# Kernel tuning notes

Measured on AMD Instinct MI355X. Metric: run time of the kernel, lower is better.

Reference implementation:

```python
import jax, jax.numpy as jnp
import numpy as np

DIM = 768
NUM_HEADS = 8
HEAD_DIM = DIM // NUM_HEADS
SCALE = HEAD_DIM ** -0.5


def setup_inputs() -> dict:
    key = jax.random.key(0)
    k1, k2, k3, k4 = jax.random.split(key, 4)
    B, C, H, W = 8, DIM, 32, 32
    x = jax.random.normal(k1, (B, C, H, W), dtype=jnp.float32)
    # torch Linear stores weight as (out, in); y = x @ W.T + b
    w_qkv = jax.random.normal(k2, (3 * DIM, DIM), dtype=jnp.float32) * (DIM ** -0.5)
    w_proj = jax.random.normal(k3, (DIM, DIM), dtype=jnp.float32) * (DIM ** -0.5)
    b_proj = jax.random.normal(k4, (DIM,), dtype=jnp.float32) * 0.02
    return {"x": x, "w_qkv": w_qkv, "w_proj": w_proj, "b_proj": b_proj}


def reference(x, w_qkv, w_proj, b_proj):
    B, C, H, W = x.shape
    N = H * W
    nh, hd = NUM_HEADS, HEAD_DIM
    # (B, C, H, W) -> (B, N, C)
    tokens = x.reshape(B, C, N).transpose(0, 2, 1)
    qkv = tokens @ w_qkv.T  # (B, N, 3C), no bias (qkv_bias=False)
    qkv = qkv.reshape(B, N, 3, nh, hd).transpose(2, 0, 3, 1, 4)  # (3, B, nh, N, hd)
    q, k, v = qkv[0], qkv[1], qkv[2]
    attn = jnp.einsum('bhnd,bhmd->bhnm', q, k) * SCALE
    attn = jax.nn.softmax(attn, axis=-1)  # attn_drop=0.0 (eval)
    out = jnp.einsum('bhnm,bhmd->bhnd', attn, v)  # (B, nh, N, hd)
    out = out.transpose(0, 2, 1, 3).reshape(B, N, C)
    out = out @ w_proj.T + b_proj  # proj_drop=0.0
    return out.transpose(0, 2, 1).reshape(B, C, H, W)
```

## Files before the change

### kernel.cpp

```cpp
#include <hip/hip_runtime.h>

typedef short s16x8 __attribute__((ext_vector_type(8)));
typedef short s16x4 __attribute__((ext_vector_type(4)));
typedef float f32x4 __attribute__((ext_vector_type(4)));
typedef int   i32x4 __attribute__((ext_vector_type(4)));
typedef unsigned u32x2 __attribute__((ext_vector_type(2)));

#define SCALE_F 0.10206207261596577f
#define KLOG2E  0.14724444f
#define DEFER_THR 11.5415603f

__device__ __forceinline__ unsigned short f2bf(float f) {
  unsigned u = __builtin_bit_cast(unsigned, f);
  u += 0x7fffu + ((u >> 16) & 1u);
  return (unsigned short)(u >> 16);
}
__device__ __forceinline__ unsigned cvt_pk_bf16(float a, float b) {
  unsigned r;
  asm("v_cvt_pk_bf16_f32 %0, %1, %2" : "=v"(r) : "v"(a), "v"(b));
  return r;
}
__device__ __forceinline__ float exp2_fast(float x) {
  float r;
  asm("v_exp_f32 %0, %1" : "=v"(r) : "v"(x));
  return r;
}

#define MFMA16(a, b, c) __builtin_amdgcn_mfma_f32_16x16x32_bf16((a), (b), (c), 0, 0, 0)

__device__ __forceinline__ void gl_lds16(const unsigned short* g, unsigned short* l) {
  __builtin_amdgcn_global_load_lds(
      (const __attribute__((address_space(1))) void*)g,
      (__attribute__((address_space(3))) void*)l, 16, 0, 0);
}

__global__ __launch_bounds__(256) void cvt_bf16_kernel(const float* __restrict__ src,
                                                       unsigned short* __restrict__ dst, int n4) {
  int i = blockIdx.x * 256 + threadIdx.x;
  if (i >= n4) return;
  f32x4 v = reinterpret_cast<const f32x4*>(src)[i];
  s16x4 o;
  o[0] = (short)f2bf(v[0]); o[1] = (short)f2bf(v[1]);
  o[2] = (short)f2bf(v[2]); o[3] = (short)f2bf(v[3]);
  reinterpret_cast<s16x4*>(dst)[i] = o;
}

__global__ __launch_bounds__(256) void transpose_x_kernel(const float* __restrict__ x,
                                                          unsigned short* __restrict__ tokens) {
  __shared__ float t[32][33];
  const int ct = blockIdx.x * 32, nt = blockIdx.y * 32, b = blockIdx.z;
  const int tx = threadIdx.x, ty = threadIdx.y;
  const float* xp = x + (size_t)b * 768 * 1024;
#pragma unroll
  for (int r = 0; r < 4; ++r) {
    int c = ty + r * 8;
    t[c][tx] = xp[(size_t)(ct + c) * 1024 + nt + tx];
  }
  __syncthreads();
  unsigned short* tp = tokens + (size_t)b * 1024 * 768;
#pragma unroll
  for (int r = 0; r < 4; ++r) {
    int n = ty + r * 8;
    tp[(size_t)(nt + n) * 768 + ct + tx] = f2bf(t[tx][n]);
  }
}

__global__ __launch_bounds__(512, 4) void qkv_gemm_kernel(const unsigned short* __restrict__ A,
                                                          const unsigned short* __restrict__ Bt,
                                                          unsigned short* __restrict__ Qo,
                                                          unsigned short* __restrict__ Ko,
                                                          unsigned short* __restrict__ Vt) {
  __shared__ unsigned short lds[36864];
  const int tid = threadIdx.x;
  const int wave = tid >> 6, lane = tid & 63;
  const int wm = wave >> 1, wn = wave & 1;
  const int lr = lane & 15, lg = lane >> 4;
  const int bid = blockIdx.x;
  const int xcd = bid & 7, idx = bid >> 3;
  const int m0 = (xcd * 4 + idx / 18) * 256;
  const int n0 = (idx % 18) * 128;

  const int srow = tid >> 2, sslot = tid & 3;

  f32x4 acc[4][4] = {};

#define STAGE_KT(ktv, bb)                                                       \
  {                                                                             \
    unsigned short* lb = lds + (bb) * 12288;                                    \
    _Pragma("unroll")                                                           \
    for (int rr = 0; rr < 2; ++rr) {                                            \
      const int row = rr * 128 + srow;                                          \
      const int c = sslot ^ ((row >> 1) & 3);                                   \
      gl_lds16(A + (size_t)(m0 + row) * 768 + (ktv) * 32 + c * 8,               \
               lb + rr * 4096 + wave * 512);                                    \
    }                                                                           \
    {                                                                           \
      const int c = sslot ^ ((srow >> 1) & 3);                                  \
      gl_lds16(Bt + (size_t)(n0 + srow) * 768 + (ktv) * 32 + c * 8,             \
               lb + 8192 + wave * 512);                                         \
    }                                                                           \
  }

  STAGE_KT(0, 0)
  STAGE_KT(1, 1)
  asm volatile("s_waitcnt vmcnt(3)" ::: "memory");
  __builtin_amdgcn_s_barrier();

  int cb = 0;
  for (int kt = 0; kt < 24; ++kt) {
    unsigned short* curb = lds + cb * 12288;
    s16x8 af[4], bf[4];
#pragma unroll
    for (int mi = 0; mi < 4; ++mi) {
      const int row = wm * 64 + mi * 16 + lr;
      af[mi] = *reinterpret_cast<const s16x8*>(
          &curb[row * 32 + ((lg ^ ((row >> 1) & 3)) * 8)]);
    }
#pragma unroll
    for (int ni = 0; ni < 4; ++ni) {
      const int row = wn * 64 + ni * 16 + lr;
      bf[ni] = *reinterpret_cast<const s16x8*>(
          &curb[8192 + row * 32 + ((lg ^ ((row >> 1) & 3)) * 8)]);
    }
    if (kt < 22) {
      const int sb = (cb == 0) ? 2 : cb - 1;
      STAGE_KT(kt + 2, sb)
    }
    __builtin_amdgcn_s_barrier();
    asm volatile("s_waitcnt lgkmcnt(0)" ::: "memory");
    __builtin_amdgcn_sched_barrier(0);
    __builtin_amdgcn_s_setprio(1);
#pragma unroll
    for (int mi = 0; mi < 4; ++mi)
#pragma unroll
      for (int ni = 0; ni < 4; ++ni)
        acc[mi][ni] = MFMA16(af[mi], bf[ni], acc[mi][ni]);
    __builtin_amdgcn_s_setprio(0);
    if (kt < 22) {
      asm volatile("s_waitcnt vmcnt(3)" ::: "memory");
    } else if (kt == 22) {
      asm volatile("s_waitcnt vmcnt(0)" ::: "memory");
    }
    __builtin_amdgcn_s_barrier();
    cb = (cb == 2) ? 0 : cb + 1;
  }
#undef STAGE_KT

  const int colbase = n0 + wn * 64;
  const int ttype = colbase / 768;
  if (ttype == 2) {
#pragma unroll
    for (int ni = 0; ni < 4; ++ni) {
      const int cc = colbase + ni * 16 + lr - 2 * 768;
      const int h = cc / 96, d = cc - h * 96;
#pragma unroll
      for (int mi = 0; mi < 4; ++mi) {
        const int gm = m0 + wm * 64 + mi * 16 + lg * 4;
        const int b = gm >> 10, n = gm & 1023;
        const int np = (n & ~31) | (((n >> 2) & 3) << 3) | (((n >> 4) & 1) << 2);
        u32x2 p2;
        p2[0] = cvt_pk_bf16(acc[mi][ni][0], acc[mi][ni][1]);
        p2[1] = cvt_pk_bf16(acc[mi][ni][2], acc[mi][ni][3]);
        *reinterpret_cast<s16x4*>(Vt + ((size_t)(b * 8 + h) * 96 + d) * 1024 + np) =
            __builtin_bit_cast(s16x4, p2);
      }
    }
  } else {
    unsigned short* W = lds + wave * 4096;
    unsigned short* dstbuf = (ttype == 0) ? Qo : Ko;
#pragma unroll
    for (int mi = 0; mi < 4; ++mi)
#pragma unroll
      for (int ni = 0; ni < 4; ++ni) {
        const int cc = ni * 16 + lr;
        const int ch = cc >> 3, wi = cc & 7;
#pragma unroll
        for (int j = 0; j < 4; ++j) {
          const int r = mi * 16 + lg * 4 + j;
          W[r * 64 + ((ch ^ (r & 7)) * 8) + wi] = f2bf(acc[mi][ni][j]);
        }
      }
    asm volatile("s_waitcnt lgkmcnt(0)" ::: "memory");
    __builtin_amdgcn_sched_barrier(0);
#pragma unroll
    for (int i = 0; i < 8; ++i) {
      const int r = i * 8 + (lane >> 3), c = lane & 7;
      s16x8 v8 = *reinterpret_cast<const s16x8*>(&W[r * 64 + ((c ^ (r & 7)) * 8)]);
      const int cc = colbase + c * 8 - ttype * 768;
      const int h = cc / 96, d = cc - h * 96;
      const int gm = m0 + wm * 64 + r;
      const int b = gm >> 10, n = gm & 1023;
      *reinterpret_cast<s16x8*>(dstbuf + ((size_t)(b * 8 + h) * 1024 + n) * 96 + d) = v8;
    }
  }
}

__device__ __forceinline__ void stage128(const unsigned short* __restrict__ A,
                                         const unsigned short* __restrict__ Bt,
                                         unsigned short* lA, unsigned short* lB,
                                         int m0, int n0, int k0, int tid, int wave) {
  const int r2 = tid >> 2, s = tid & 3;
#pragma unroll
  for (int i = 0; i < 2; ++i) {
    const int row = i * 64 + r2;
    const int c = s ^ ((row >> 1) & 3);
    gl_lds16(A + (size_t)(m0 + row) * 768 + k0 + c * 8, lA + i * 2048 + wave * 512);
    gl_lds16(Bt + (size_t)(n0 + row) * 768 + k0 + c * 8, lB + i * 2048 + wave * 512);
  }
}

#define GEMM128_LOOP(A, Bt)                                                             \
  stage128(A, Bt, lA, lB, m0, n0, 0, tid, wave);                                        \
  __syncthreads();                                                                      \
  for (int t = 0; t < 24; ++t) {                                                        \
    const int cur = t & 1;                                                              \
    if (t < 23)                                                                         \
      stage128(A, Bt, lA + (cur ^ 1) * 4096, lB + (cur ^ 1) * 4096, m0, n0,             \
               (t + 1) * 32, tid, wave);                                                \
    s16x8 af[4], bf[4];                                                                 \
    _Pragma("unroll")                                                                   \
    for (int mi = 0; mi < 4; ++mi) {                                                    \
      const int row = wr * 64 + mi * 16 + lr;                                           \
      af[mi] = *reinterpret_cast<const s16x8*>(                                         \
          &lA[cur * 4096 + row * 32 + ((lg ^ ((row >> 1) & 3)) * 8)]);                  \
    }                                                                                   \
    _Pragma("unroll")                                                                   \
    for (int ni = 0; ni < 4; ++ni) {                                                    \
      const int row = wc * 64 + ni * 16 + lr;                                           \
      bf[ni] = *reinterpret_cast<const s16x8*>(                                         \
          &lB[cur * 4096 + row * 32 + ((lg ^ ((row >> 1) & 3)) * 8)]);                  \
    }                                                                                   \
    _Pragma("unroll")                                                                   \
    for (int mi = 0; mi < 4; ++mi)                                                      \
      _Pragma("unroll")                                                                 \
      for (int ni = 0; ni < 4; ++ni)                                                    \
        acc[mi][ni] = MFMA16(af[mi], bf[ni], acc[mi][ni]);                              \
    __syncthreads();                                                                    \
  }

__global__ __launch_bounds__(256, 4) void proj_gemm_kernel(const unsigned short* __restrict__ A,
                                                           const unsigned short* __restrict__ Bt,
                                                           const float* __restrict__ bias,
                                                           float* __restrict__ out) {
  __shared__ unsigned short lds_all[16384];
  unsigned short* lA = lds_all;
  unsigned short* lB = lds_all + 8192;

  const int tid = threadIdx.x;
  const int wave = tid >> 6, lane = tid & 63;
  const int wr = wave >> 1, wc = wave & 1;
  const int lr = lane & 15, lg = lane >> 4;
  const int bid = blockIdx.x;
  const int xcd = bid & 7, idx = bid >> 3;
  const int m0 = (xcd * 8 + idx / 6) * 128;
  const int n0 = (idx % 6) * 128;

  f32x4 acc[4][4] = {};
  GEMM128_LOOP(A, Bt)

#pragma unroll
  for (int ni = 0; ni < 4; ++ni) {
    const int col = n0 + wc * 64 + ni * 16 + lr;
    const float bv = bias[col];
#pragma unroll
    for (int mi = 0; mi < 4; ++mi) {
      const int gm = m0 + wr * 64 + mi * 16 + lg * 4;
      const int b = gm >> 10, n = gm & 1023;
      f32x4 v;
#pragma unroll
      for (int j = 0; j < 4; ++j) v[j] = acc[mi][ni][j] + bv;
      *reinterpret_cast<f32x4*>(out + (size_t)b * 768 * 1024 + (size_t)col * 1024 + n) = v;
    }
  }
}

__global__ __launch_bounds__(512, 4) void attn_kernel(const unsigned short* __restrict__ Q,
                                                      const unsigned short* __restrict__ K,
                                                      const unsigned short* __restrict__ Vt,
                                                      unsigned short* __restrict__ Ao) {
  __shared__ unsigned short lds[2][12288];

  const int f = blockIdx.x;
  const int xcd = f & 7;
  const int g = (f >> 3) + xcd * 64;
  const int bh = g >> 3, qb = g & 7;

  const int tid = threadIdx.x, wave = tid >> 6, lane = tid & 63;
  const int lr = lane & 15, lg = lane >> 4;
  const int klo = (lr >> 1) & 3;

  const unsigned short* Qp = Q + (size_t)bh * 1024 * 96;
  const unsigned short* Kp = K + (size_t)bh * 1024 * 96;
  const unsigned short* Vp = Vt + (size_t)bh * 96 * 1024;

  const int qrow = qb * 128 + wave * 16 + lr;
  s16x8 qreg[3];
#pragma unroll
  for (int kd = 0; kd < 3; ++kd)
    qreg[kd] = *reinterpret_cast<const s16x8*>(Qp + (size_t)qrow * 96 + kd * 32 + lg * 8);

  float m2 = -1e30f, l_r = 0.f;
  f32x4 oacc[6] = {};

#define STAGE(bufi, kv0)                                                              \
  {                                                                                   \
    _Pragma("unroll")                                                                 \
    for (int i = 0; i < 3; ++i) {                                                     \
      const int wl = wave + 8 * i;                                                    \
      if (wl < 12) {                                                                  \
        const int kd = wl >> 2, rg = wl & 3;                                          \
        const int row = rg * 16 + (lane >> 2);                                        \
        const int c8 = (lane & 3) ^ ((row >> 1) & 3);                                 \
        gl_lds16(Kp + (size_t)((kv0) + row) * 96 + kd * 32 + c8 * 8,                  \
                 &lds[bufi][0] + kd * 2048 + rg * 512);                               \
      } else {                                                                        \
        const int v = wl - 12;                                                        \
        const int gs = v / 6, rg = v - gs * 6;                                        \
        const int drow = rg * 16 + (lane >> 2);                                       \
        const int c8 = (lane & 3) ^ ((drow >> 1) & 3);                                \
        gl_lds16(Vp + (size_t)drow * 1024 + (kv0) + gs * 32 + c8 * 8,                 \
                 &lds[bufi][0] + 6144 + gs * 3072 + rg * 512);                        \
      }                                                                               \
    }                                                                                 \
  }

  STAGE(0, 0);
  __syncthreads();

  for (int gt = 0; gt < 16; ++gt) {
    const int buf = gt & 1;
    if (gt < 15) STAGE(buf ^ 1, (gt + 1) * 64);

    f32x4 sacc[4] = {};
    __builtin_amdgcn_s_setprio(1);
#pragma unroll
    for (int c = 0; c < 4; ++c) {
#pragma unroll
      for (int kd = 0; kd < 3; ++kd) {
        s16x8 kf = *reinterpret_cast<const s16x8*>(
            &lds[buf][kd * 2048 + (c * 16 + lr) * 32 + ((lg ^ klo) * 8)]);
        sacc[c] = MFMA16(kf, qreg[kd], sacc[c]);
      }
    }
    __builtin_amdgcn_s_setprio(0);

    float mx = fmaxf(fmaxf(sacc[0][0], sacc[0][1]), fmaxf(sacc[0][2], sacc[0][3]));
#pragma unroll
    for (int c = 1; c < 4; ++c)
      mx = fmaxf(mx, fmaxf(fmaxf(sacc[c][0], sacc[c][1]), fmaxf(sacc[c][2], sacc[c][3])));
    mx = fmaxf(mx, __shfl_xor(mx, 16));
    mx = fmaxf(mx, __shfl_xor(mx, 32));
    const float mc = mx * KLOG2E;
    if (!__all(mc - m2 <= DEFER_THR)) {
      const float m2n = fmaxf(m2, mc);
      const float rsc = exp2_fast(m2 - m2n);
      l_r *= rsc;
#pragma unroll
      for (int dt = 0; dt < 6; ++dt) oacc[dt] *= rsc;
      m2 = m2n;
    }
    float ts = 0.f;
    unsigned pk[4][2];
#pragma unroll
    for (int c = 0; c < 4; ++c) {
      float p0 = exp2_fast(__builtin_fmaf(sacc[c][0], KLOG2E, -m2));
      float p1 = exp2_fast(__builtin_fmaf(sacc[c][1], KLOG2E, -m2));
      float p2 = exp2_fast(__builtin_fmaf(sacc[c][2], KLOG2E, -m2));
      float p3 = exp2_fast(__builtin_fmaf(sacc[c][3], KLOG2E, -m2));
      ts += (p0 + p1) + (p2 + p3);
      pk[c][0] = cvt_pk_bf16(p0, p1);
      pk[c][1] = cvt_pk_bf16(p2, p3);
    }
    ts += __shfl_xor(ts, 16);
    ts += __shfl_xor(ts, 32);
    l_r += ts;

    __builtin_amdgcn_s_setprio(1);
#pragma unroll
    for (int gs = 0; gs < 2; ++gs) {
      i32x4 bi;
      bi[0] = (int)pk[2 * gs][0];
      bi[1] = (int)pk[2 * gs][1];
      bi[2] = (int)pk[2 * gs + 1][0];
      bi[3] = (int)pk[2 * gs + 1][1];
      s16x8 pf = __builtin_bit_cast(s16x8, bi);
#pragma unroll
      for (int dt = 0; dt < 6; ++dt) {
        s16x8 vf = *reinterpret_cast<const s16x8*>(
            &lds[buf][6144 + gs * 3072 + (dt * 16 + lr) * 32 + ((lg ^ klo) * 8)]);
        oacc[dt] = MFMA16(vf, pf, oacc[dt]);
      }
    }
    __builtin_amdgcn_s_setprio(0);
    __syncthreads();
  }

  const float invl = 1.0f / l_r;
  const int b_ = bh >> 3, h_ = bh & 7;
  unsigned short* orow = Ao + (size_t)(b_ * 1024 + qrow) * 768 + h_ * 96;
#pragma unroll
  for (int dt = 0; dt < 6; ++dt) {
    u32x2 p2;
    p2[0] = cvt_pk_bf16(oacc[dt][0] * invl, oacc[dt][1] * invl);
    p2[1] = cvt_pk_bf16(oacc[dt][2] * invl, oacc[dt][3] * invl);
    *reinterpret_cast<s16x4*>(orow + dt * 16 + lg * 4) = __builtin_bit_cast(s16x4, p2);
  }
#undef STAGE
}

extern "C" void kernel_launch(void* const* d_in, const int* in_sizes, int n_in,
                              void* d_out, int out_size, void* d_ws, size_t ws_size,
                              hipStream_t stream) {
  const float* x = (const float*)d_in[0];
  const float* wqkv = (const float*)d_in[1];
  const float* wproj = (const float*)d_in[2];
  const float* bproj = (const float*)d_in[3];
  float* out = (float*)d_out;

  unsigned short* ws = (unsigned short*)d_ws;
  unsigned short* tokens = ws;
  unsigned short* wqkv_b = tokens + 8192 * 768;
  unsigned short* wproj_b = wqkv_b + 2304 * 768;
  unsigned short* Qb = wproj_b + 768 * 768;
  unsigned short* Kb = Qb + 64 * 1024 * 96;
  unsigned short* Vb = Kb + 64 * 1024 * 96;
  unsigned short* Ab = Vb + 64 * 1024 * 96;

  cvt_bf16_kernel<<<1728, 256, 0, stream>>>(wqkv, wqkv_b, 2304 * 768 / 4);
  cvt_bf16_kernel<<<576, 256, 0, stream>>>(wproj, wproj_b, 768 * 768 / 4);
  transpose_x_kernel<<<dim3(24, 32, 8), dim3(32, 8), 0, stream>>>(x, tokens);
  qkv_gemm_kernel<<<576, 512, 0, stream>>>(tokens, wqkv_b, Qb, Kb, Vb);
  attn_kernel<<<512, 512, 0, stream>>>(Qb, Kb, Vb, Ab);
  proj_gemm_kernel<<<384, 256, 0, stream>>>(Ab, wproj_b, bproj, out);
}
```

Before: 116.7 us.

## Process two query tiles per wave in attention to reuse K/V fragments

```diff
diff --git a/kernel.cpp b/kernel.cpp
--- a/kernel.cpp
+++ b/kernel.cpp
@@ -209,35 +209,6 @@
   }
 }
 
-#define GEMM128_LOOP(A, Bt)                                                             \
-  stage128(A, Bt, lA, lB, m0, n0, 0, tid, wave);                                        \
-  __syncthreads();                                                                      \
-  for (int t = 0; t < 24; ++t) {                                                        \
-    const int cur = t & 1;                                                              \
-    if (t < 23)                                                                         \
-      stage128(A, Bt, lA + (cur ^ 1) * 4096, lB + (cur ^ 1) * 4096, m0, n0,             \
-               (t + 1) * 32, tid, wave);                                                \
-    s16x8 af[4], bf[4];                                                                 \
-    _Pragma("unroll")                                                                   \
-    for (int mi = 0; mi < 4; ++mi) {                                                    \
-      const int row = wr * 64 + mi * 16 + lr;                                           \
-      af[mi] = *reinterpret_cast<const s16x8*>(                                         \
-          &lA[cur * 4096 + row * 32 + ((lg ^ ((row >> 1) & 3)) * 8)]);                  \
-    }                                                                                   \
-    _Pragma("unroll")                                                                   \
-    for (int ni = 0; ni < 4; ++ni) {                                                    \
-      const int row = wc * 64 + ni * 16 + lr;                                           \
-      bf[ni] = *reinterpret_cast<const s16x8*>(                                         \
-          &lB[cur * 4096 + row * 32 + ((lg ^ ((row >> 1) & 3)) * 8)]);                  \
-    }                                                                                   \
-    _Pragma("unroll")                                                                   \
-    for (int mi = 0; mi < 4; ++mi)                                                      \
-      _Pragma("unroll")                                                                 \
-      for (int ni = 0; ni < 4; ++ni)                                                    \
-        acc[mi][ni] = MFMA16(af[mi], bf[ni], acc[mi][ni]);                              \
-    __syncthreads();                                                                    \
-  }
-
 __global__ __launch_bounds__(256, 4) void proj_gemm_kernel(const unsigned short* __restrict__ A,
                                                            const unsigned short* __restrict__ Bt,
                                                            const float* __restrict__ bias,
@@ -256,7 +227,33 @@
   const int n0 = (idx % 6) * 128;
 
   f32x4 acc[4][4] = {};
-  GEMM128_LOOP(A, Bt)
+  stage128(A, Bt, lA, lB, m0, n0, 0, tid, wave);
+  __syncthreads();
+  for (int t = 0; t < 24; ++t) {
+    const int cur = t & 1;
+    if (t < 23)
+      stage128(A, Bt, lA + (cur ^ 1) * 4096, lB + (cur ^ 1) * 4096, m0, n0,
+               (t + 1) * 32, tid, wave);
+    s16x8 af[4], bf[4];
+#pragma unroll
+    for (int mi = 0; mi < 4; ++mi) {
+      const int row = wr * 64 + mi * 16 + lr;
+      af[mi] = *reinterpret_cast<const s16x8*>(
+          &lA[cur * 4096 + row * 32 + ((lg ^ ((row >> 1) & 3)) * 8)]);
+    }
+#pragma unroll
+    for (int ni = 0; ni < 4; ++ni) {
+      const int row = wc * 64 + ni * 16 + lr;
+      bf[ni] = *reinterpret_cast<const s16x8*>(
+          &lB[cur * 4096 + row * 32 + ((lg ^ ((row >> 1) & 3)) * 8)]);
+    }
+#pragma unroll
+    for (int mi = 0; mi < 4; ++mi)
+#pragma unroll
+      for (int ni = 0; ni < 4; ++ni)
+        acc[mi][ni] = MFMA16(af[mi], bf[ni], acc[mi][ni]);
+    __syncthreads();
+  }
 
 #pragma unroll
   for (int ni = 0; ni < 4; ++ni) {
@@ -274,7 +271,7 @@
   }
 }
 
-__global__ __launch_bounds__(512, 4) void attn_kernel(const unsigned short* __restrict__ Q,
+__global__ __launch_bounds__(256, 2) void attn_kernel(const unsigned short* __restrict__ Q,
                                                       const unsigned short* __restrict__ K,
                                                       const unsigned short* __restrict__ Vt,
                                                       unsigned short* __restrict__ Ao) {
@@ -293,20 +290,23 @@
   const unsigned short* Kp = K + (size_t)bh * 1024 * 96;
   const unsigned short* Vp = Vt + (size_t)bh * 96 * 1024;
 
-  const int qrow = qb * 128 + wave * 16 + lr;
-  s16x8 qreg[3];
-#pragma unroll
-  for (int kd = 0; kd < 3; ++kd)
-    qreg[kd] = *reinterpret_cast<const s16x8*>(Qp + (size_t)qrow * 96 + kd * 32 + lg * 8);
-
-  float m2 = -1e30f, l_r = 0.f;
-  f32x4 oacc[6] = {};
+  s16x8 qreg[3][2];
+#pragma unroll
+  for (int u = 0; u < 2; ++u) {
+    const int qrow = qb * 128 + wave * 32 + u * 16 + lr;
+#pragma unroll
+    for (int kd = 0; kd < 3; ++kd)
+      qreg[kd][u] = *reinterpret_cast<const s16x8*>(Qp + (size_t)qrow * 96 + kd * 32 + lg * 8);
+  }
+
+  float m2[2] = {-1e30f, -1e30f}, l_r[2] = {0.f, 0.f};
+  f32x4 oacc[6][2] = {};
 
 #define STAGE(bufi, kv0)                                                              \
   {                                                                                   \
     _Pragma("unroll")                                                                 \
-    for (int i = 0; i < 3; ++i) {                                                     \
-      const int wl = wave + 8 * i;                                                    \
+    for (int i = 0; i < 6; ++i) {                                                     \
+      const int wl = wave + 4 * i;                                                    \
       if (wl < 12) {                                                                  \
         const int kd = wl >> 2, rg = wl & 3;                                          \
         const int row = rg * 16 + (lane >> 2);                                        \
@@ -331,79 +331,97 @@
     const int buf = gt & 1;
     if (gt < 15) STAGE(buf ^ 1, (gt + 1) * 64);
 
-    f32x4 sacc[4] = {};
+    f32x4 sacc[4][2] = {};
     __builtin_amdgcn_s_setprio(1);
 #pragma unroll
     for (int c = 0; c < 4; ++c) {
-#pragma unroll
-      for (int kd = 0; kd < 3; ++kd) {
-        s16x8 kf = *reinterpret_cast<const s16x8*>(
+      s16x8 kf[3];
+#pragma unroll
+      for (int kd = 0; kd < 3; ++kd)
+        kf[kd] = *reinterpret_cast<const s16x8*>(
             &lds[buf][kd * 2048 + (c * 16 + lr) * 32 + ((lg ^ klo) * 8)]);
-        sacc[c] = MFMA16(kf, qreg[kd], sacc[c]);
-      }
+#pragma unroll
+      for (int kd = 0; kd < 3; ++kd)
+#pragma unroll
+        for (int u = 0; u < 2; ++u)
+          sacc[c][u] = MFMA16(kf[kd], qreg[kd][u], sacc[c][u]);
     }
     __builtin_amdgcn_s_setprio(0);
 
-    float mx = fmaxf(fmaxf(sacc[0][0], sacc[0][1]), fmaxf(sacc[0][2], sacc[0][3]));
-#pragma unroll
-    for (int c = 1; c < 4; ++c)
-      mx = fmaxf(mx, fmaxf(fmaxf(sacc[c][0], sacc[c][1]), fmaxf(sacc[c][2], sacc[c][3])));
-    mx = fmaxf(mx, __shfl_xor(mx, 16));
-    mx = fmaxf(mx, __shfl_xor(mx, 32));
-    const float mc = mx * KLOG2E;
-    if (!__all(mc - m2 <= DEFER_THR)) {
-      const float m2n = fmaxf(m2, mc);
-      const float rsc = exp2_fast(m2 - m2n);
-      l_r *= rsc;
-#pragma unroll
-      for (int dt = 0; dt < 6; ++dt) oacc[dt] *= rsc;
-      m2 = m2n;
-    }
-    float ts = 0.f;
-    unsigned pk[4][2];
-#pragma unroll
-    for (int c = 0; c < 4; ++c) {
-      float p0 = exp2_fast(__builtin_fmaf(sacc[c][0], KLOG2E, -m2));
-      float p1 = exp2_fast(__builtin_fmaf(sacc[c][1], KLOG2E, -m2));
-      float p2 = exp2_fast(__builtin_fmaf(sacc[c][2], KLOG2E, -m2));
-      float p3 = exp2_fast(__builtin_fmaf(sacc[c][3], KLOG2E, -m2));
-      ts += (p0 + p1) + (p2 + p3);
-      pk[c][0] = cvt_pk_bf16(p0, p1);
-      pk[c][1] = cvt_pk_bf16(p2, p3);
-    }
-    ts += __shfl_xor(ts, 16);
-    ts += __shfl_xor(ts, 32);
-    l_r += ts;
+    unsigned pk[2][4][2];
+#pragma unroll
+    for (int u = 0; u < 2; ++u) {
+      float mx = fmaxf(fmaxf(sacc[0][u][0], sacc[0][u][1]), fmaxf(sacc[0][u][2], sacc[0][u][3]));
+#pragma unroll
+      for (int c = 1; c < 4; ++c)
+        mx = fmaxf(mx, fmaxf(fmaxf(sacc[c][u][0], sacc[c][u][1]),
+                             fmaxf(sacc[c][u][2], sacc[c][u][3])));
+      mx = fmaxf(mx, __shfl_xor(mx, 16));
+      mx = fmaxf(mx, __shfl_xor(mx, 32));
+      const float mc = mx * KLOG2E;
+      if (!__all(mc - m2[u] <= DEFER_THR)) {
+        const float m2n = fmaxf(m2[u], mc);
+        const float rsc = exp2_fast(m2[u] - m2n);
+        l_r[u] *= rsc;
+#pragma unroll
+        for (int dt = 0; dt < 6; ++dt) oacc[dt][u] *= rsc;
+        m2[u] = m2n;
+      }
+      float ts = 0.f;
+#pragma unroll
+      for (int c = 0; c < 4; ++c) {
+        float p0 = exp2_fast(__builtin_fmaf(sacc[c][u][0], KLOG2E, -m2[u]));
+        float p1 = exp2_fast(__builtin_fmaf(sacc[c][u][1], KLOG2E, -m2[u]));
+        float p2 = exp2_fast(__builtin_fmaf(sacc[c][u][2], KLOG2E, -m2[u]));
+        float p3 = exp2_fast(__builtin_fmaf(sacc[c][u][3], KLOG2E, -m2[u]));
+        ts += (p0 + p1) + (p2 + p3);
+        pk[u][c][0] = cvt_pk_bf16(p0, p1);
+        pk[u][c][1] = cvt_pk_bf16(p2, p3);
+      }
+      ts += __shfl_xor(ts, 16);
+      ts += __shfl_xor(ts, 32);
+      l_r[u] += ts;
+    }
 
     __builtin_amdgcn_s_setprio(1);
 #pragma unroll
     for (int gs = 0; gs < 2; ++gs) {
-      i32x4 bi;
-      bi[0] = (int)pk[2 * gs][0];
-      bi[1] = (int)pk[2 * gs][1];
-      bi[2] = (int)pk[2 * gs + 1][0];
-      bi[3] = (int)pk[2 * gs + 1][1];
-      s16x8 pf = __builtin_bit_cast(s16x8, bi);
+      s16x8 pf[2];
+#pragma unroll
+      for (int u = 0; u < 2; ++u) {
+        i32x4 bi;
+        bi[0] = (int)pk[u][2 * gs][0];
+        bi[1] = (int)pk[u][2 * gs][1];
+        bi[2] = (int)pk[u][2 * gs + 1][0];
+        bi[3] = (int)pk[u][2 * gs + 1][1];
+        pf[u] = __builtin_bit_cast(s16x8, bi);
+      }
 #pragma unroll
       for (int dt = 0; dt < 6; ++dt) {
         s16x8 vf = *reinterpret_cast<const s16x8*>(
             &lds[buf][6144 + gs * 3072 + (dt * 16 + lr) * 32 + ((lg ^ klo) * 8)]);
-        oacc[dt] = MFMA16(vf, pf, oacc[dt]);
+#pragma unroll
+        for (int u = 0; u < 2; ++u)
+          oacc[dt][u] = MFMA16(vf, pf[u], oacc[dt][u]);
       }
     }
     __builtin_amdgcn_s_setprio(0);
     __syncthreads();
   }
 
-  const float invl = 1.0f / l_r;
   const int b_ = bh >> 3, h_ = bh & 7;
-  unsigned short* orow = Ao + (size_t)(b_ * 1024 + qrow) * 768 + h_ * 96;
-#pragma unroll
-  for (int dt = 0; dt < 6; ++dt) {
-    u32x2 p2;
-    p2[0] = cvt_pk_bf16(oacc[dt][0] * invl, oacc[dt][1] * invl);
-    p2[1] = cvt_pk_bf16(oacc[dt][2] * invl, oacc[dt][3] * invl);
-    *reinterpret_cast<s16x4*>(orow + dt * 16 + lg * 4) = __builtin_bit_cast(s16x4, p2);
+#pragma unroll
+  for (int u = 0; u < 2; ++u) {
+    const float invl = 1.0f / l_r[u];
+    const int qrow = qb * 128 + wave * 32 + u * 16 + lr;
+    unsigned short* orow = Ao + (size_t)(b_ * 1024 + qrow) * 768 + h_ * 96;
+#pragma unroll
+    for (int dt = 0; dt < 6; ++dt) {
+      u32x2 p2;
+      p2[0] = cvt_pk_bf16(oacc[dt][u][0] * invl, oacc[dt][u][1] * invl);
+      p2[1] = cvt_pk_bf16(oacc[dt][u][2] * invl, oacc[dt][u][3] * invl);
+      *reinterpret_cast<s16x4*>(orow + dt * 16 + lg * 4) = __builtin_bit_cast(s16x4, p2);
+    }
   }
 #undef STAGE
 }
@@ -430,6 +448,6 @@
   cvt_bf16_kernel<<<576, 256, 0, stream>>>(wproj, wproj_b, 768 * 768 / 4);
   transpose_x_kernel<<<dim3(24, 32, 8), dim3(32, 8), 0, stream>>>(x, tokens);
   qkv_gemm_kernel<<<576, 512, 0, stream>>>(tokens, wqkv_b, Qb, Kb, Vb);
-  attn_kernel<<<512, 512, 0, stream>>>(Qb, Kb, Vb, Ab);
+  attn_kernel<<<512, 256, 0, stream>>>(Qb, Kb, Vb, Ab);
   proj_gemm_kernel<<<384, 256, 0, stream>>>(Ab, wproj_b, bproj, out);
 }
```

After: 117.3 us. No clear change (+0.5%).
